# Kernel tuning notes

Hardware: AMD Instinct MI355X
Metric: run time of the kernel (lower is better)

Reference implementation:

```python
import jax, jax.numpy as jnp
import numpy as np
import math

D_KEY = 64
D_VALUE = 64
NUM_HEADS = 16
D_MODEL = D_VALUE * NUM_HEADS  # 1024


def setup_inputs() -> dict:
    key = jax.random.key(0)
    ks = jax.random.split(key, 5)
    B, N = 2, 2048
    s = 1.0 / math.sqrt(D_MODEL)
    return {
        "x": jax.random.normal(ks[0], (B, N, D_MODEL), dtype=jnp.float32),
        "Wq": jax.random.normal(ks[1], (D_MODEL, D_KEY * NUM_HEADS), dtype=jnp.float32) * s,
        "Wk": jax.random.normal(ks[2], (D_MODEL, D_KEY * NUM_HEADS), dtype=jnp.float32) * s,
        "Wv": jax.random.normal(ks[3], (D_MODEL, D_MODEL), dtype=jnp.float32) * s,
        "Wp": jax.random.normal(ks[4], (D_MODEL, D_MODEL), dtype=jnp.float32) * s,
    }


def reference(x, Wq, Wk, Wv, Wp):
    # x: [B, N, d_model]. Equivalent to the original block-diagonal concat trick:
    # off-diagonal blocks are -inf, so softmax over the key axis reduces to
    # independent per-head softmax attention.
    B, N, D = x.shape
    H, K, V = NUM_HEADS, D_KEY, D_VALUE
    scale = 1.0 / math.sqrt(K)
    q = (x @ Wq).reshape(B, N, H, K)
    k = (x @ Wk).reshape(B, N, H, K)
    v = (x @ Wv).reshape(B, N, H, V)
    scores = jnp.einsum("bnhk,bmhk->bhnm", q, k) * scale  # [B,H,N,N]
    attn = jax.nn.softmax(scores, axis=-1)
    out = jnp.einsum("bhnm,bmhv->bnhv", attn, v).reshape(B, N, D)
    return x + out @ Wp
```

## Files before the change

kernel.cpp:

```cpp
#include <hip/hip_runtime.h>

typedef float f32x4 __attribute__((ext_vector_type(4)));
typedef __bf16 bf16x8 __attribute__((ext_vector_type(8)));

#define DEV static __device__ __forceinline__

DEV ushort f2bf(float f) {
  unsigned u = __builtin_bit_cast(unsigned, f);
  u += 0x7FFFu + ((u >> 16) & 1u);
  return (ushort)(u >> 16);
}

DEV bf16x8 ld_frag(const ushort* p) {
  return __builtin_bit_cast(bf16x8, *reinterpret_cast<const int4*>(p));
}

DEV bf16x8 ld_lds(const ushort* base, int byte_off) {
  return __builtin_bit_cast(bf16x8,
      *reinterpret_cast<const int4*>(reinterpret_cast<const char*>(base) + byte_off));
}

DEV int swz(int row, int col_byte) { return row * 128 + (col_byte ^ ((row & 7) << 4)); }

DEV float fast_exp2(float x) {
  float r;
  asm("v_exp_f32 %0, %1" : "=v"(r) : "v"(x));
  return r;
}

DEV unsigned cvt_pk_bf16(float lo, float hi) {
  unsigned r;
  asm("v_cvt_pk_bf16_f32 %0, %1, %2" : "=v"(r) : "v"(lo), "v"(hi));
  return r;
}

DEV void gload16(const ushort* g, ushort* l) {
  __builtin_amdgcn_global_load_lds(
      (const __attribute__((address_space(1))) unsigned int*)g,
      (__attribute__((address_space(3))) unsigned int*)l, 16, 0, 0);
}


__global__ __launch_bounds__(256) void prep(const float* __restrict__ x,
                                            const float* __restrict__ w0,
                                            const float* __restrict__ w1,
                                            const float* __restrict__ w2,
                                            const float* __restrict__ w3,
                                            ushort* __restrict__ xb,
                                            ushort* __restrict__ wt) {
  __shared__ float tile[32][33];
  const int z = blockIdx.z;
  const int tx = threadIdx.x, ty = threadIdx.y;
  if (z < 4) {
    const float* w = z == 0 ? w0 : z == 1 ? w1 : z == 2 ? w2 : w3;
    ushort* out = wt + (size_t)z * 1024 * 1024;
    const int n0 = blockIdx.x * 32, k0 = blockIdx.y * 32;
    float4 v = *reinterpret_cast<const float4*>(&w[(size_t)(k0 + ty) * 1024 + n0 + tx * 4]);
    tile[ty][tx * 4 + 0] = v.x;
    tile[ty][tx * 4 + 1] = v.y;
    tile[ty][tx * 4 + 2] = v.z;
    tile[ty][tx * 4 + 3] = v.w;
    __syncthreads();
    ushort4 o = make_ushort4(f2bf(tile[tx * 4 + 0][ty]), f2bf(tile[tx * 4 + 1][ty]),
                             f2bf(tile[tx * 4 + 2][ty]), f2bf(tile[tx * 4 + 3][ty]));
    *reinterpret_cast<ushort4*>(&out[(size_t)(n0 + ty) * 1024 + k0 + tx * 4]) = o;
  } else {
    const int blk = ((z - 4) * 32 + blockIdx.y) * 32 + blockIdx.x;
    const int tid = ty * 8 + tx;
    const int i = blk * 256 + tid;
    float4 v = reinterpret_cast<const float4*>(x)[i];
    ushort4 o = make_ushort4(f2bf(v.x), f2bf(v.y), f2bf(v.z), f2bf(v.w));
    reinterpret_cast<ushort4*>(xb)[i] = o;
  }
}

__global__ __launch_bounds__(256) void gemm_qkv(const ushort* __restrict__ xb,
                                                const ushort* __restrict__ wT,
                                                ushort* __restrict__ q, ushort* __restrict__ k,
                                                ushort* __restrict__ vt) {
  __shared__ ushort a_lds[128 * 64];
  __shared__ ushort b_lds[3][64 * 64];
  const int fid = blockIdx.x;
  const int wid = (fid & 7) * 64 + (fid >> 3);
  const int row0 = (wid >> 4) * 128, col0 = (wid & 15) * 64;
  const int tid = threadIdx.x;
  const int lane = tid & 63;
  const int w = tid >> 6, wr = w >> 1, wc = w & 1;
  const int lg = lane >> 4, l15 = lane & 15;
  const int sr8 = lane >> 3;
  const int scol = ((lane & 7) ^ sr8) << 3;
  const ushort* ga = xb + (size_t)(row0 + w * 32 + sr8) * 1024 + scol;
  const ushort* gb[3];
#pragma unroll
  for (int z = 0; z < 3; ++z)
    gb[z] = wT + (size_t)z * 1024 * 1024 + (size_t)(col0 + w * 16 + sr8) * 1024 + scol;

  f32x4 acc[3][4][2];
#pragma unroll
  for (int z = 0; z < 3; ++z)
#pragma unroll
    for (int ai = 0; ai < 4; ++ai)
#pragma unroll
      for (int bj = 0; bj < 2; ++bj) acc[z][ai][bj] = f32x4{0.f, 0.f, 0.f, 0.f};

  for (int kt = 0; kt < 1024; kt += 64) {
    __syncthreads();
#pragma unroll
    for (int p = 0; p < 4; ++p)
      gload16(ga + kt + (size_t)(p * 8) * 1024, a_lds + (w * 32 + p * 8) * 64);
#pragma unroll
    for (int z = 0; z < 3; ++z)
#pragma unroll
      for (int p = 0; p < 2; ++p)
        gload16(gb[z] + kt + (size_t)(p * 8) * 1024, b_lds[z] + (w * 16 + p * 8) * 64);
    __syncthreads();
    bf16x8 af[4][2];
#pragma unroll
    for (int kk = 0; kk < 2; ++kk)
#pragma unroll
      for (int i = 0; i < 4; ++i)
        af[i][kk] = ld_lds(a_lds, swz(wr * 64 + i * 16 + l15, kk * 64 + lg * 16));
#pragma unroll
    for (int z = 0; z < 3; ++z) {
      bf16x8 bfr[2][2];
#pragma unroll
      for (int kk = 0; kk < 2; ++kk)
#pragma unroll
        for (int j = 0; j < 2; ++j)
          bfr[j][kk] = ld_lds(b_lds[z], swz(wc * 32 + j * 16 + l15, kk * 64 + lg * 16));
#pragma unroll
      for (int kk = 0; kk < 2; ++kk)
#pragma unroll
        for (int ai = 0; ai < 4; ++ai)
#pragma unroll
          for (int bj = 0; bj < 2; ++bj)
            acc[z][ai][bj] = __builtin_amdgcn_mfma_f32_16x16x32_bf16(af[ai][kk], bfr[bj][kk],
                                                                     acc[z][ai][bj], 0, 0, 0);
    }
  }

#pragma unroll
  for (int z = 0; z < 2; ++z) {
    ushort* out = z == 0 ? q : k;
    const float sc = z == 0 ? 0.125f * 1.4426950408889634f : 1.0f;
#pragma unroll
    for (int ai = 0; ai < 4; ++ai)
#pragma unroll
      for (int bj = 0; bj < 2; ++bj)
#pragma unroll
        for (int r = 0; r < 4; ++r) {
          int orow = row0 + wr * 64 + ai * 16 + lg * 4 + r;
          int ocol = col0 + wc * 32 + bj * 16 + l15;
          out[(size_t)orow * 1024 + ocol] = f2bf(acc[z][ai][bj][r] * sc);
        }
  }
#pragma unroll
  for (int ai = 0; ai < 4; ++ai)
#pragma unroll
    for (int bj = 0; bj < 2; ++bj) {
      int orow = row0 + wr * 64 + ai * 16 + lg * 4;
      int ocol = col0 + wc * 32 + bj * 16 + l15;
      int bb = orow >> 11, n = orow & 2047;
      ushort4 pk = make_ushort4(f2bf(acc[2][ai][bj][0]), f2bf(acc[2][ai][bj][1]),
                                f2bf(acc[2][ai][bj][2]), f2bf(acc[2][ai][bj][3]));
      *reinterpret_cast<ushort4*>(vt + ((size_t)(bb * 1024 + ocol)) * 2048 + n) = pk;
    }
}

__global__ __launch_bounds__(256) void gemm_out(const ushort* __restrict__ ob,
                                                const ushort* __restrict__ wpT,
                                                const float* __restrict__ x,
                                                float* __restrict__ y) {
  __shared__ ushort a_lds[64 * 64], b_lds[64 * 64];
  const int fid = blockIdx.x;
  const int wid = (fid & 7) * 128 + (fid >> 3);
  const int row0 = (wid >> 4) * 64, col0 = (wid & 15) * 64;
  const int tid = threadIdx.x;
  const int lane = tid & 63;
  const int w = tid >> 6, wr = w >> 1, wc = w & 1;
  const int lg = lane >> 4, l15 = lane & 15;
  const int sr8 = lane >> 3;
  const int scol = ((lane & 7) ^ sr8) << 3;
  const ushort* ga = ob + (size_t)(row0 + w * 16 + sr8) * 1024 + scol;
  const ushort* gb = wpT + (size_t)(col0 + w * 16 + sr8) * 1024 + scol;

  f32x4 acc[2][2];
#pragma unroll
  for (int ai = 0; ai < 2; ++ai)
#pragma unroll
    for (int bj = 0; bj < 2; ++bj) acc[ai][bj] = f32x4{0.f, 0.f, 0.f, 0.f};

  for (int kt = 0; kt < 1024; kt += 64) {
    __syncthreads();
#pragma unroll
    for (int p = 0; p < 2; ++p) {
      gload16(ga + kt + (size_t)(p * 8) * 1024, a_lds + (w * 16 + p * 8) * 64);
      gload16(gb + kt + (size_t)(p * 8) * 1024, b_lds + (w * 16 + p * 8) * 64);
    }
    __syncthreads();
    bf16x8 af[2][2], bfr[2][2];
#pragma unroll
    for (int kk = 0; kk < 2; ++kk) {
#pragma unroll
      for (int i = 0; i < 2; ++i) {
        af[i][kk] = ld_lds(a_lds, swz(wr * 32 + i * 16 + l15, kk * 64 + lg * 16));
        bfr[i][kk] = ld_lds(b_lds, swz(wc * 32 + i * 16 + l15, kk * 64 + lg * 16));
      }
    }
#pragma unroll
    for (int kk = 0; kk < 2; ++kk)
#pragma unroll
      for (int ai = 0; ai < 2; ++ai)
#pragma unroll
        for (int bj = 0; bj < 2; ++bj)
          acc[ai][bj] = __builtin_amdgcn_mfma_f32_16x16x32_bf16(af[ai][kk], bfr[bj][kk],
                                                                acc[ai][bj], 0, 0, 0);
  }

#pragma unroll
  for (int ai = 0; ai < 2; ++ai)
#pragma unroll
    for (int bj = 0; bj < 2; ++bj)
#pragma unroll
      for (int r = 0; r < 4; ++r) {
        int orow = row0 + wr * 32 + ai * 16 + lg * 4 + r;
        int ocol = col0 + wc * 32 + bj * 16 + l15;
        size_t idx = (size_t)orow * 1024 + ocol;
        y[idx] = x[idx] + acc[ai][bj][r];
      }
}

__global__ __launch_bounds__(256) void attn(const ushort* __restrict__ qg,
                                            const ushort* __restrict__ kg,
                                            const ushort* __restrict__ vtg,
                                            ushort* __restrict__ og) {
  __shared__ ushort k_lds[4 * 64 * 64];
  __shared__ ushort v_lds[4 * 64 * 64];
  const int fid = blockIdx.x;
  const int wid = (fid & 7) * 64 + (fid >> 3);
  const int bh = wid >> 4, q0 = wid & 15;
  const int b = bh >> 4, h = bh & 15;
  const int n0 = q0 * 128;
  const int tid = threadIdx.x, lane = tid & 63, w = tid >> 6;
  const int lg = lane >> 4, l15 = lane & 15;

  bf16x8 qf[2][2];
#pragma unroll
  for (int qi = 0; qi < 2; ++qi)
#pragma unroll
    for (int d32 = 0; d32 < 2; ++d32)
      qf[qi][d32] = ld_frag(qg + (size_t)(b * 2048 + n0 + w * 32 + qi * 16 + l15) * 1024 +
                            h * 64 + d32 * 32 + lg * 8);

  f32x4 o[2][4];
#pragma unroll
  for (int qi = 0; qi < 2; ++qi)
#pragma unroll
    for (int bj = 0; bj < 4; ++bj) o[qi][bj] = f32x4{0.f, 0.f, 0.f, 0.f};
  f32x4 ssum[2] = {f32x4{0.f, 0.f, 0.f, 0.f}, f32x4{0.f, 0.f, 0.f, 0.f}};

  const int sr8 = lane >> 3;
  const int scol = ((lane & 7) ^ sr8) << 3;
  const ushort* kbase = kg + (size_t)(b * 2048 + w * 16 + sr8) * 1024 + h * 64 + scol;
  const ushort* vbase = vtg + (size_t)(b * 1024 + h * 64 + w * 16 + sr8) * 2048 + scol;

  auto stage_sub = [&](ushort* kdst, ushort* vdst, int kv0) {
#pragma unroll
    for (int p = 0; p < 2; ++p) {
      gload16(kbase + (size_t)(kv0 + p * 8) * 1024, kdst + (w * 16 + p * 8) * 64);
      gload16(vbase + (size_t)(p * 8) * 2048 + kv0, vdst + (w * 16 + p * 8) * 64);
    }
  };
  auto stage2 = [&](int buf, int kv0) {
    stage_sub(k_lds + (2 * buf) * 4096, v_lds + (2 * buf) * 4096, kv0);
    stage_sub(k_lds + (2 * buf + 1) * 4096, v_lds + (2 * buf + 1) * 4096, kv0 + 64);
  };

  const int4 ones4 = make_int4(0x3F803F80, 0x3F803F80, 0x3F803F80, 0x3F803F80);
  const bf16x8 onesf = __builtin_bit_cast(bf16x8, ones4);

  auto qk_sub = [&](const ushort* kb, f32x4 s[2][4]) {
#pragma unroll
    for (int qi = 0; qi < 2; ++qi)
#pragma unroll
      for (int kj = 0; kj < 4; ++kj) s[qi][kj] = f32x4{0.f, 0.f, 0.f, 0.f};
#pragma unroll
    for (int d32 = 0; d32 < 2; ++d32)
#pragma unroll
      for (int kj = 0; kj < 4; ++kj) {
        bf16x8 kf = ld_lds(kb, swz(kj * 16 + l15, d32 * 64 + lg * 16));
        s[0][kj] = __builtin_amdgcn_mfma_f32_16x16x32_bf16(kf, qf[0][d32], s[0][kj], 0, 0, 0);
        s[1][kj] = __builtin_amdgcn_mfma_f32_16x16x32_bf16(kf, qf[1][d32], s[1][kj], 0, 0, 0);
      }
  };

  auto exp_pack = [&](f32x4 s[2][4], bf16x8 pa[2][2]) {
#pragma unroll
    for (int qi = 0; qi < 2; ++qi) {
      unsigned pk[4][2];
#pragma unroll
      for (int kj = 0; kj < 4; ++kj) {
        float p0 = fast_exp2(s[qi][kj][0]);
        float p1 = fast_exp2(s[qi][kj][1]);
        float p2 = fast_exp2(s[qi][kj][2]);
        float p3 = fast_exp2(s[qi][kj][3]);
        pk[kj][0] = cvt_pk_bf16(p0, p1);
        pk[kj][1] = cvt_pk_bf16(p2, p3);
      }
#pragma unroll
      for (int k32 = 0; k32 < 2; ++k32) {
        unsigned x0 = pk[2 * k32][0], y0 = pk[2 * k32 + 1][0];
        unsigned x1 = pk[2 * k32][1], y1 = pk[2 * k32 + 1][1];
        asm("v_permlane32_swap_b32 %0, %1" : "+v"(x0), "+v"(y0));
        asm("v_permlane32_swap_b32 %0, %1" : "+v"(x1), "+v"(y1));
        asm("v_permlane16_swap_b32 %0, %1" : "+v"(x0), "+v"(y0));
        asm("v_permlane16_swap_b32 %0, %1" : "+v"(x1), "+v"(y1));
        int4 fr = make_int4(x0, x1, y0, y1);
        pa[qi][k32] = __builtin_bit_cast(bf16x8, fr);
      }
    }
  };

  auto pv_only = [&](const ushort* vb, bf16x8 pa[2][2]) {
#pragma unroll
    for (int qi = 0; qi < 2; ++qi) {
      ssum[qi] = __builtin_amdgcn_mfma_f32_16x16x32_bf16(pa[qi][0], onesf, ssum[qi], 0, 0, 0);
      ssum[qi] = __builtin_amdgcn_mfma_f32_16x16x32_bf16(pa[qi][1], onesf, ssum[qi], 0, 0, 0);
    }
#pragma unroll
    for (int k32 = 0; k32 < 2; ++k32)
#pragma unroll
      for (int bj = 0; bj < 4; ++bj) {
        bf16x8 vf = ld_lds(vb, swz(bj * 16 + l15, k32 * 64 + lg * 16));
        o[0][bj] = __builtin_amdgcn_mfma_f32_16x16x32_bf16(pa[0][k32], vf, o[0][bj], 0, 0, 0);
        o[1][bj] = __builtin_amdgcn_mfma_f32_16x16x32_bf16(pa[1][k32], vf, o[1][bj], 0, 0, 0);
      }
  };

  auto body2 = [&](int buf) {
    const ushort* kb0 = k_lds + (2 * buf) * 4096;
    const ushort* kb1 = k_lds + (2 * buf + 1) * 4096;
    const ushort* vb0 = v_lds + (2 * buf) * 4096;
    const ushort* vb1 = v_lds + (2 * buf + 1) * 4096;
    f32x4 s0[2][4], s1[2][4];
    bf16x8 pa0[2][2], pa1[2][2];
    qk_sub(kb0, s0);
    qk_sub(kb1, s1);
    exp_pack(s0, pa0);
    pv_only(vb0, pa0);
    exp_pack(s1, pa1);
    pv_only(vb1, pa1);
    __builtin_amdgcn_sched_group_barrier(0x020, 8, 0);
    __builtin_amdgcn_sched_group_barrier(0x100, 8, 0);
    __builtin_amdgcn_sched_group_barrier(0x008, 16, 0);
    __builtin_amdgcn_sched_group_barrier(0x100, 8, 0);
#pragma unroll
    for (int i = 0; i < 16; ++i) {
      __builtin_amdgcn_sched_group_barrier(0x008, 1, 0);
      __builtin_amdgcn_sched_group_barrier(0x002, 4, 0);
    }
    __builtin_amdgcn_sched_group_barrier(0x100, 8, 0);
#pragma unroll
    for (int i = 0; i < 20; ++i) {
      __builtin_amdgcn_sched_group_barrier(0x008, 1, 0);
      __builtin_amdgcn_sched_group_barrier(0x002, 3, 0);
    }
    __builtin_amdgcn_sched_group_barrier(0x100, 8, 0);
    __builtin_amdgcn_sched_group_barrier(0x008, 20, 0);
  };

  stage2(0, 0);
  __syncthreads();

  for (int tt = 0; tt < 8; ++tt) {
    stage2(1, (2 * tt + 1) * 128);
    body2(0);
    __syncthreads();
    if (tt < 7) stage2(0, (2 * tt + 2) * 128);
    body2(1);
    __syncthreads();
  }

#pragma unroll
  for (int qi = 0; qi < 2; ++qi) {
    f32x4 inv;
#pragma unroll
    for (int r = 0; r < 4; ++r) inv[r] = 1.0f / ssum[qi][r];
#pragma unroll
    for (int bj = 0; bj < 4; ++bj)
#pragma unroll
      for (int r = 0; r < 4; ++r) {
        int n = n0 + w * 32 + qi * 16 + lg * 4 + r;
        og[(size_t)(b * 2048 + n) * 1024 + h * 64 + bj * 16 + l15] = f2bf(o[qi][bj][r] * inv[r]);
      }
  }
}


extern "C" void kernel_launch(void* const* d_in, const int* in_sizes, int n_in,
                              void* d_out, int out_size, void* d_ws, size_t ws_size,
                              hipStream_t stream) {
  const float* x = (const float*)d_in[0];
  const float* Wq = (const float*)d_in[1];
  const float* Wk = (const float*)d_in[2];
  const float* Wv = (const float*)d_in[3];
  const float* Wp = (const float*)d_in[4];
  float* y = (float*)d_out;

  char* ws = (char*)d_ws;
  ushort* xb = (ushort*)(ws);
  ushort* wT = (ushort*)(ws + (8ull << 20));
  ushort* qw = (ushort*)(ws + (16ull << 20));
  ushort* kw = (ushort*)(ws + (24ull << 20));
  ushort* vtw = (ushort*)(ws + (32ull << 20));
  ushort* ow = (ushort*)(ws);

  prep<<<dim3(32, 32, 8), dim3(8, 32), 0, stream>>>(x, Wq, Wk, Wv, Wp, xb, wT);
  gemm_qkv<<<512, 256, 0, stream>>>(xb, wT, qw, kw, vtw);
  attn<<<512, 256, 0, stream>>>(qw, kw, vtw, ow);
  gemm_out<<<1024, 256, 0, stream>>>(ow, wT + (3u << 20), x, y);
}
```

Before: 102.8 us.

## Double-buffer LDS tiles in QKV and output projection GEMMs

Both GEMM kernels now use two LDS buffers, issuing the global-to-LDS loads for the next K tile before computing on the current one. This halves the barriers per K step and is meant to hide global load latency behind MFMA work. It doubles LDS usage per block (to about 80KB for gemm_qkv), which may reduce occupancy. Correctness depends on gload16 completing before the following barrier.

```diff
diff --git a/kernel.cpp b/kernel.cpp
--- a/kernel.cpp
+++ b/kernel.cpp
@@ -78,8 +78,8 @@
                                                 const ushort* __restrict__ wT,
                                                 ushort* __restrict__ q, ushort* __restrict__ k,
                                                 ushort* __restrict__ vt) {
-  __shared__ ushort a_lds[128 * 64];
-  __shared__ ushort b_lds[3][64 * 64];
+  __shared__ ushort a_lds[2][128 * 64];
+  __shared__ ushort b_lds[2][3][64 * 64];
   const int fid = blockIdx.x;
   const int wid = (fid & 7) * 64 + (fid >> 3);
   const int row0 = (wid >> 4) * 128, col0 = (wid & 15) * 64;
@@ -103,23 +103,24 @@
 #pragma unroll
       for (int bj = 0; bj < 2; ++bj) acc[z][ai][bj] = f32x4{0.f, 0.f, 0.f, 0.f};
 
-  for (int kt = 0; kt < 1024; kt += 64) {
-    __syncthreads();
+  auto stage = [&](int buf, int kt) {
 #pragma unroll
     for (int p = 0; p < 4; ++p)
-      gload16(ga + kt + (size_t)(p * 8) * 1024, a_lds + (w * 32 + p * 8) * 64);
+      gload16(ga + kt + (size_t)(p * 8) * 1024, a_lds[buf] + (w * 32 + p * 8) * 64);
 #pragma unroll
     for (int z = 0; z < 3; ++z)
 #pragma unroll
       for (int p = 0; p < 2; ++p)
-        gload16(gb[z] + kt + (size_t)(p * 8) * 1024, b_lds[z] + (w * 16 + p * 8) * 64);
-    __syncthreads();
+        gload16(gb[z] + kt + (size_t)(p * 8) * 1024, b_lds[buf][z] + (w * 16 + p * 8) * 64);
+  };
+
+  auto compute = [&](int buf) {
     bf16x8 af[4][2];
 #pragma unroll
     for (int kk = 0; kk < 2; ++kk)
 #pragma unroll
       for (int i = 0; i < 4; ++i)
-        af[i][kk] = ld_lds(a_lds, swz(wr * 64 + i * 16 + l15, kk * 64 + lg * 16));
+        af[i][kk] = ld_lds(a_lds[buf], swz(wr * 64 + i * 16 + l15, kk * 64 + lg * 16));
 #pragma unroll
     for (int z = 0; z < 3; ++z) {
       bf16x8 bfr[2][2];
@@ -127,7 +128,7 @@
       for (int kk = 0; kk < 2; ++kk)
 #pragma unroll
         for (int j = 0; j < 2; ++j)
-          bfr[j][kk] = ld_lds(b_lds[z], swz(wc * 32 + j * 16 + l15, kk * 64 + lg * 16));
+          bfr[j][kk] = ld_lds(b_lds[buf][z], swz(wc * 32 + j * 16 + l15, kk * 64 + lg * 16));
 #pragma unroll
       for (int kk = 0; kk < 2; ++kk)
 #pragma unroll
@@ -137,6 +138,17 @@
             acc[z][ai][bj] = __builtin_amdgcn_mfma_f32_16x16x32_bf16(af[ai][kk], bfr[bj][kk],
                                                                      acc[z][ai][bj], 0, 0, 0);
     }
+  };
+
+  stage(0, 0);
+  __syncthreads();
+  for (int t = 0; t < 8; ++t) {
+    stage(1, (2 * t + 1) * 64);
+    compute(0);
+    __syncthreads();
+    if (t < 7) stage(0, (2 * t + 2) * 64);
+    compute(1);
+    __syncthreads();
   }
 
 #pragma unroll
@@ -171,7 +183,7 @@
                                                 const ushort* __restrict__ wpT,
                                                 const float* __restrict__ x,
                                                 float* __restrict__ y) {
-  __shared__ ushort a_lds[64 * 64], b_lds[64 * 64];
+  __shared__ ushort a_lds[2][64 * 64], b_lds[2][64 * 64];
   const int fid = blockIdx.x;
   const int wid = (fid & 7) * 128 + (fid >> 3);
   const int row0 = (wid >> 4) * 64, col0 = (wid & 15) * 64;
@@ -190,21 +202,22 @@
 #pragma unroll
     for (int bj = 0; bj < 2; ++bj) acc[ai][bj] = f32x4{0.f, 0.f, 0.f, 0.f};
 
-  for (int kt = 0; kt < 1024; kt += 64) {
-    __syncthreads();
+  auto stage = [&](int buf, int kt) {
 #pragma unroll
     for (int p = 0; p < 2; ++p) {
-      gload16(ga + kt + (size_t)(p * 8) * 1024, a_lds + (w * 16 + p * 8) * 64);
-      gload16(gb + kt + (size_t)(p * 8) * 1024, b_lds + (w * 16 + p * 8) * 64);
-    }
-    __syncthreads();
+      gload16(ga + kt + (size_t)(p * 8) * 1024, a_lds[buf] + (w * 16 + p * 8) * 64);
+      gload16(gb + kt + (size_t)(p * 8) * 1024, b_lds[buf] + (w * 16 + p * 8) * 64);
+    }
+  };
+
+  auto compute = [&](int buf) {
     bf16x8 af[2][2], bfr[2][2];
 #pragma unroll
     for (int kk = 0; kk < 2; ++kk) {
 #pragma unroll
       for (int i = 0; i < 2; ++i) {
-        af[i][kk] = ld_lds(a_lds, swz(wr * 32 + i * 16 + l15, kk * 64 + lg * 16));
-        bfr[i][kk] = ld_lds(b_lds, swz(wc * 32 + i * 16 + l15, kk * 64 + lg * 16));
+        af[i][kk] = ld_lds(a_lds[buf], swz(wr * 32 + i * 16 + l15, kk * 64 + lg * 16));
+        bfr[i][kk] = ld_lds(b_lds[buf], swz(wc * 32 + i * 16 + l15, kk * 64 + lg * 16));
       }
     }
 #pragma unroll
@@ -215,6 +228,17 @@
         for (int bj = 0; bj < 2; ++bj)
           acc[ai][bj] = __builtin_amdgcn_mfma_f32_16x16x32_bf16(af[ai][kk], bfr[bj][kk],
                                                                 acc[ai][bj], 0, 0, 0);
+  };
+
+  stage(0, 0);
+  __syncthreads();
+  for (int t = 0; t < 8; ++t) {
+    stage(1, (2 * t + 1) * 64);
+    compute(0);
+    __syncthreads();
+    if (t < 7) stage(0, (2 * t + 2) * 64);
+    compute(1);
+    __syncthreads();
   }
 
 #pragma unroll
```

Result: slower. 126.1 us (+22.7%).
